# Kernel optimization log

Hardware: AMD Instinct MI355X
Metric: run time of the kernel (lower is better)

Reference implementation:

```python
import jax, jax.numpy as jnp
import numpy as np

Na, Nn, E, D = 8192, 65536, 262144, 128
NB = 2  # n_blk Att blocks
EPS = 1e-5  # torch GroupNorm default eps


def _gn(x, g, b):
    # GroupNorm with 1 group on [N, C]: normalize each row over channels
    mu = jnp.mean(x, axis=-1, keepdims=True)
    var = jnp.mean((x - mu) ** 2, axis=-1, keepdims=True)
    return (x - mu) * jax.lax.rsqrt(var + EPS) * g + b


def setup_inputs() -> dict:
    key = jax.random.key(0)
    ks = jax.random.split(key, 28)
    s = 0.05
    inp = {
        'actors': jax.random.normal(ks[0], (Na, D), jnp.float32),
        'nodes': jax.random.normal(ks[1], (Nn, D), jnp.float32),
        'actor_ctrs': jax.random.uniform(ks[2], (Na, 2), jnp.float32, 0.0, 100.0),
        'node_ctrs': jax.random.uniform(ks[3], (Nn, 2), jnp.float32, 0.0, 100.0),
        'hi': jax.random.randint(ks[4], (E,), 0, Na, jnp.int32),
        'wi': jax.random.randint(ks[5], (E,), 0, Nn, jnp.int32),
        # stacked params for NB=2 Att blocks
        'dist0_W': jax.random.normal(ks[6], (NB, D, 2), jnp.float32) * s,
        'dist0_b': jnp.zeros((NB, D), jnp.float32),
        'dist1_W': jax.random.normal(ks[7], (NB, D, D), jnp.float32) * s,
        'dist1_g': jnp.ones((NB, D), jnp.float32),
        'dist1_b': jnp.zeros((NB, D), jnp.float32),
        'query_W': jax.random.normal(ks[8], (NB, D, D), jnp.float32) * s,
        'query_g': jnp.ones((NB, D), jnp.float32),
        'query_b': jnp.zeros((NB, D), jnp.float32),
        'ctx0_W': jax.random.normal(ks[9], (NB, D, 3 * D), jnp.float32) * s,
        'ctx0_g': jnp.ones((NB, D), jnp.float32),
        'ctx0_b': jnp.zeros((NB, D), jnp.float32),
        'ctx1_W': jax.random.normal(ks[10], (NB, D, D), jnp.float32) * s,
        'agt_W': jax.random.normal(ks[11], (NB, D, D), jnp.float32) * s,
        'norm_g': jnp.ones((NB, D), jnp.float32),
        'norm_b': jnp.zeros((NB, D), jnp.float32),
        'lin_W': jax.random.normal(ks[12], (NB, D, D), jnp.float32) * s,
        'lin_g': jnp.ones((NB, D), jnp.float32),
        'lin_b': jnp.zeros((NB, D), jnp.float32),
    }
    return inp


def reference(actors, nodes, actor_ctrs, node_ctrs, hi, wi,
              dist0_W, dist0_b, dist1_W, dist1_g, dist1_b,
              query_W, query_g, query_b,
              ctx0_W, ctx0_g, ctx0_b, ctx1_W, agt_W,
              norm_g, norm_b, lin_W, lin_g, lin_b):
    for i in range(NB):
        res = actors
        # dist MLP on edge displacement vectors [E, 2]
        d = actor_ctrs[hi] - node_ctrs[wi]
        d = jax.nn.relu(d @ dist0_W[i].T + dist0_b[i])
        d = jax.nn.relu(_gn(d @ dist1_W[i].T, dist1_g[i], dist1_b[i]))
        # query from target agents, gathered per-edge
        q = jax.nn.relu(_gn(actors @ query_W[i].T, query_g[i], query_b[i]))[hi]
        c = nodes[wi]
        m = jnp.concatenate([d, q, c], axis=-1)  # [E, 3D]
        m = jax.nn.relu(_gn(m @ ctx0_W[i].T, ctx0_g[i], ctx0_b[i]))
        m = m @ ctx1_W[i].T  # [E, D]
        # scatter-add messages into agents (index_add_)
        a = actors @ agt_W[i].T
        a = a.at[hi].add(m)
        a = jax.nn.relu(_gn(a, norm_g[i], norm_b[i]))
        a = _gn(a @ lin_W[i].T, lin_g[i], lin_b[i])  # act=False
        actors = jax.nn.relu(a + res)
    return actors
```

## Files before the change

kernel.cpp:

```cpp
#include <hip/hip_runtime.h>
#include <hip/hip_bf16.h>

typedef __hip_bfloat16 bf16;
typedef __attribute__((ext_vector_type(8))) short bf16x8;
typedef __attribute__((ext_vector_type(4))) float f32x4;

constexpr int DD = 128;
constexpr int NAC = 8192;
constexpr int NND = 65536;
constexpr int NEG = 262144;
constexpr int AP = 136;
constexpr float GN_EPS = 1e-5f;

#define DEVINL __device__ __attribute__((always_inline)) static inline

DEVINL float bf2f(short s) {
    return __uint_as_float(((unsigned int)(unsigned short)s) << 16);
}

DEVINL void stage_half(const bf16* __restrict__ src, bf16* buf, int wid, int lane)
{
    const bf16* g = src + (size_t)(wid * 4) * 512 + lane * 8;
    bf16* l = buf + (wid * 4) * 512;
    #pragma unroll
    for (int i = 0; i < 4; i++) {
        __builtin_amdgcn_global_load_lds(
            (const __attribute__((address_space(1))) void*)(g + i * 512),
            (__attribute__((address_space(3))) void*)(l + i * 512),
            16, 0, 0);
    }
}

DEVINL void stage_h16(const bf16* __restrict__ src, bf16* buf, int lane)
{
    const bf16* g = src + lane * 8;
    #pragma unroll
    for (int i = 0; i < 16; i++) {
        __builtin_amdgcn_global_load_lds(
            (const __attribute__((address_space(1))) void*)(g + i * 512),
            (__attribute__((address_space(3))) void*)(buf + i * 512),
            16, 0, 0);
    }
}

DEVINL void compute_half(const bf16* buf, const bf16* Abuf,
                         f32x4 (&acc)[2][8], int eb, int quad, int l16, int lane, int kh)
{
    #pragma unroll
    for (int ks2 = 0; ks2 < 2; ks2++) {
        int kk = kh + ks2 * 32;
        bf16x8 a0 = *(const bf16x8*)(Abuf + (eb + l16) * AP + kk + quad * 8);
        bf16x8 a1 = *(const bf16x8*)(Abuf + (eb + 16 + l16) * AP + kk + quad * 8);
        #pragma unroll
        for (int nt = 0; nt < 8; nt++) {
            bf16x8 b = *(const bf16x8*)(buf + ((ks2 * 8 + nt) * 64 + lane) * 8);
            acc[0][nt] = __builtin_amdgcn_mfma_f32_16x16x32_bf16(a0, b, acc[0][nt], 0, 0, 0);
            acc[1][nt] = __builtin_amdgcn_mfma_f32_16x16x32_bf16(a1, b, acc[1][nt], 0, 0, 0);
        }
    }
}

DEVINL void zero_acc(f32x4 (&acc)[2][8])
{
    #pragma unroll
    for (int i = 0; i < 2; i++)
        #pragma unroll
        for (int j = 0; j < 8; j++)
            acc[i][j] = f32x4{0.f, 0.f, 0.f, 0.f};
}

DEVINL void gn_relu_to_lds(f32x4 (&acc)[2][8], const float* __restrict__ g,
                           const float* __restrict__ b, bf16* Abuf,
                           int eb, int quad, int l16)
{
    float gv[8], bv[8];
    #pragma unroll
    for (int nt = 0; nt < 8; nt++) { gv[nt] = g[nt * 16 + l16]; bv[nt] = b[nt * 16 + l16]; }
    #pragma unroll
    for (int mt = 0; mt < 2; mt++) {
        #pragma unroll
        for (int r = 0; r < 4; r++) {
            float s1 = 0.f, s2 = 0.f;
            #pragma unroll
            for (int nt = 0; nt < 8; nt++) { float v = acc[mt][nt][r]; s1 += v; s2 += v * v; }
            #pragma unroll
            for (int m = 1; m < 16; m <<= 1) { s1 += __shfl_xor(s1, m, 64); s2 += __shfl_xor(s2, m, 64); }
            float mean = s1 * (1.f / 128.f);
            float sc = rsqrtf(s2 * (1.f / 128.f) - mean * mean + GN_EPS);
            int row = eb + mt * 16 + quad * 4 + r;
            #pragma unroll
            for (int nt = 0; nt < 8; nt++) {
                float y = (acc[mt][nt][r] - mean) * sc * gv[nt] + bv[nt];
                Abuf[row * AP + nt * 16 + l16] = __float2bfloat16(fmaxf(y, 0.f));
            }
        }
    }
}

DEVINL void gn_relu_acc(f32x4 (&acc)[2][8], const float* __restrict__ g,
                        const float* __restrict__ b, int l16)
{
    float gv[8], bv[8];
    #pragma unroll
    for (int nt = 0; nt < 8; nt++) { gv[nt] = g[nt * 16 + l16]; bv[nt] = b[nt * 16 + l16]; }
    #pragma unroll
    for (int mt = 0; mt < 2; mt++) {
        #pragma unroll
        for (int r = 0; r < 4; r++) {
            float s1 = 0.f, s2 = 0.f;
            #pragma unroll
            for (int nt = 0; nt < 8; nt++) { float v = acc[mt][nt][r]; s1 += v; s2 += v * v; }
            #pragma unroll
            for (int m = 1; m < 16; m <<= 1) { s1 += __shfl_xor(s1, m, 64); s2 += __shfl_xor(s2, m, 64); }
            float mean = s1 * (1.f / 128.f);
            float sc = rsqrtf(s2 * (1.f / 128.f) - mean * mean + GN_EPS);
            #pragma unroll
            for (int nt = 0; nt < 8; nt++)
                acc[mt][nt][r] = fmaxf((acc[mt][nt][r] - mean) * sc * gv[nt] + bv[nt], 0.f);
        }
    }
}

DEVINL bf16x8 pack_row(const f32x4 (&acc)[2][8], int mt, int r)
{
    union { bf16x8 v; bf16 h[8]; } u;
    #pragma unroll
    for (int nt = 0; nt < 8; nt++) u.h[nt] = __float2bfloat16(acc[mt][nt][r]);
    return u.v;
}

__global__ void repack_w_kernel(const float* __restrict__ d1, const float* __restrict__ qw,
                                const float* __restrict__ c0, const float* __restrict__ c1,
                                const float* __restrict__ ag, const float* __restrict__ li,
                                bf16* __restrict__ Wf, int* __restrict__ cnt)
{
    int g = blockIdx.x * 256 + threadIdx.x;
    if (g < 8192) cnt[g] = 0;
    int slice = g >> 11;
    int t = g & 2047;
    int i = slice >> 3;
    int sid = slice & 7;
    int lane = t & 63, nt = (t >> 6) & 7, ks = t >> 9;
    const float* src; int stride = 128, koff = 0;
    switch (sid) {
        case 0:  src = d1 + i * 16384; break;
        case 1:  src = qw + i * 16384; break;
        case 2:  src = c0 + i * 49152; stride = 384; koff = 0;   break;
        case 3:  src = c0 + i * 49152; stride = 384; koff = 128; break;
        case 4:  src = c0 + i * 49152; stride = 384; koff = 256; break;
        case 5:  src = c1 + i * 16384; break;
        case 6:  src = ag + i * 16384; break;
        default: src = li + i * 16384; break;
    }
    int n = nt * 16 + (lane & 15);
    int k = ks * 32 + (lane >> 4) * 8;
    const float* p = src + (size_t)n * stride + koff + k;
    float4 v0 = *(const float4*)(p);
    float4 v1 = *(const float4*)(p + 4);
    union { bf16x8 v; bf16 h[8]; } u;
    u.h[0] = __float2bfloat16(v0.x); u.h[1] = __float2bfloat16(v0.y);
    u.h[2] = __float2bfloat16(v0.z); u.h[3] = __float2bfloat16(v0.w);
    u.h[4] = __float2bfloat16(v1.x); u.h[5] = __float2bfloat16(v1.y);
    u.h[6] = __float2bfloat16(v1.z); u.h[7] = __float2bfloat16(v1.w);
    *(bf16x8*)(Wf + (size_t)slice * 16384 + (size_t)t * 8) = u.v;
}

__global__ void hist_kernel(const int* __restrict__ hi, int* __restrict__ cnt)
{
    int e = blockIdx.x * blockDim.x + threadIdx.x;
    atomicAdd(&cnt[hi[e]], 1);
}

__global__ void scan_kernel(const int* __restrict__ cnt, int* __restrict__ cur)
{
    __shared__ int part[1024];
    int t = threadIdx.x;
    int local[8]; int s = 0;
    #pragma unroll
    for (int k = 0; k < 8; k++) { local[k] = cnt[t * 8 + k]; s += local[k]; }
    part[t] = s;
    __syncthreads();
    for (int d = 1; d < 1024; d <<= 1) {
        int v = (t >= d) ? part[t - d] : 0;
        __syncthreads();
        part[t] += v;
        __syncthreads();
    }
    int base = t ? part[t - 1] : 0;
    #pragma unroll
    for (int k = 0; k < 8; k++) { cur[t * 8 + k] = base; base += local[k]; }
}

__global__ void scatter_kernel(const int* __restrict__ hi, const int* __restrict__ wi,
                               const float* __restrict__ actor_ctrs, const float* __restrict__ node_ctrs,
                               int* __restrict__ cur,
                               int* __restrict__ hi_s, int* __restrict__ wi_s,
                               float2* __restrict__ dxy_s)
{
    int e = blockIdx.x * blockDim.x + threadIdx.x;
    int h = hi[e], w = wi[e];
    int p = atomicAdd(&cur[h], 1);
    hi_s[p] = h; wi_s[p] = w;
    float2 a2 = ((const float2*)actor_ctrs)[h];
    float2 n2 = ((const float2*)node_ctrs)[w];
    dxy_s[p] = float2{a2.x - n2.x, a2.y - n2.y};
}

__global__ __launch_bounds__(256, 3) void nodec_kernel(
    const float* __restrict__ nodes, const bf16* __restrict__ c0cf, bf16* __restrict__ nc)
{
    __shared__ __align__(16) bf16 Abuf[128 * AP];
    __shared__ __align__(16) bf16 Wd[8192];
    int tid = threadIdx.x, wid = tid >> 6, lane = tid & 63, quad = lane >> 4, l16 = lane & 15;
    int eb = wid * 32, r0 = blockIdx.x * 128;
    stage_half(c0cf, Wd, wid, lane);
    for (int rr = 0; rr < 32; rr++) {
        int row = r0 + eb + rr;
        float2 v = ((const float2*)(nodes + (size_t)row * DD))[lane];
        __hip_bfloat162 p; p.x = __float2bfloat16(v.x); p.y = __float2bfloat16(v.y);
        *(__hip_bfloat162*)(Abuf + (eb + rr) * AP + lane * 2) = p;
    }
    f32x4 acc[2][8]; zero_acc(acc);
    __syncthreads();
    compute_half(Wd, Abuf, acc, eb, quad, l16, lane, 0);
    __syncthreads();
    stage_half(c0cf + 8192, Wd, wid, lane);
    __syncthreads();
    compute_half(Wd, Abuf, acc, eb, quad, l16, lane, 64);
    #pragma unroll
    for (int mt = 0; mt < 2; mt++)
        #pragma unroll
        for (int r = 0; r < 4; r++) {
            int row = r0 + eb + mt * 16 + quad * 4 + r;
            *(bf16x8*)(nc + (size_t)row * DD + l16 * 8) = pack_row(acc, mt, r);
        }
}

__global__ __launch_bounds__(64) void prep_kernel(
    const float* __restrict__ actors_in,
    const bf16* __restrict__ agf, const bf16* __restrict__ qwf,
    const float* __restrict__ qg, const float* __restrict__ qb,
    const bf16* __restrict__ c0qf,
    bf16* __restrict__ qc, float* __restrict__ A_acc, float* __restrict__ M_acc)
{
    __shared__ __align__(16) bf16 Abuf[32 * AP];
    __shared__ __align__(16) bf16 Wd[8192];
    int lane = threadIdx.x, quad = lane >> 4, l16 = lane & 15;
    int r0 = blockIdx.x * 32;
    stage_h16(agf, Wd, lane);
    for (int rr = 0; rr < 32; rr++) {
        float2 v = ((const float2*)(actors_in + (size_t)(r0 + rr) * DD))[lane];
        __hip_bfloat162 p; p.x = __float2bfloat16(v.x); p.y = __float2bfloat16(v.y);
        *(__hip_bfloat162*)(Abuf + rr * AP + lane * 2) = p;
    }
    #pragma unroll
    for (int rr = 0; rr < 16; rr++) {
        int row = r0 + rr * 2 + (lane >> 5);
        ((float4*)(M_acc + (size_t)row * DD))[lane & 31] = float4{0.f, 0.f, 0.f, 0.f};
    }
    f32x4 acc[2][8];
    zero_acc(acc);
    __syncthreads();
    compute_half(Wd, Abuf, acc, 0, quad, l16, lane, 0);
    __syncthreads();
    stage_h16(agf + 8192, Wd, lane);
    __syncthreads();
    compute_half(Wd, Abuf, acc, 0, quad, l16, lane, 64);
    __syncthreads();
    stage_h16(qwf, Wd, lane);
    #pragma unroll
    for (int mt = 0; mt < 2; mt++)
        #pragma unroll
        for (int r = 0; r < 4; r++) {
            int row = r0 + mt * 16 + quad * 4 + r;
            float4 w0{acc[mt][0][r], acc[mt][1][r], acc[mt][2][r], acc[mt][3][r]};
            float4 w1{acc[mt][4][r], acc[mt][5][r], acc[mt][6][r], acc[mt][7][r]};
            float4* p = (float4*)(A_acc + (size_t)row * DD + l16 * 8);
            p[0] = w0; p[1] = w1;
        }
    zero_acc(acc);
    __syncthreads();
    compute_half(Wd, Abuf, acc, 0, quad, l16, lane, 0);
    __syncthreads();
    stage_h16(qwf + 8192, Wd, lane);
    __syncthreads();
    compute_half(Wd, Abuf, acc, 0, quad, l16, lane, 64);
    __syncthreads();
    stage_h16(c0qf, Wd, lane);
    gn_relu_to_lds(acc, qg, qb, Abuf, 0, quad, l16);
    zero_acc(acc);
    __syncthreads();
    compute_half(Wd, Abuf, acc, 0, quad, l16, lane, 0);
    __syncthreads();
    stage_h16(c0qf + 8192, Wd, lane);
    __syncthreads();
    compute_half(Wd, Abuf, acc, 0, quad, l16, lane, 64);
    #pragma unroll
    for (int mt = 0; mt < 2; mt++)
        #pragma unroll
        for (int r = 0; r < 4; r++) {
            int row = r0 + mt * 16 + quad * 4 + r;
            *(bf16x8*)(qc + (size_t)row * DD + l16 * 8) = pack_row(acc, mt, r);
        }
}

__global__ __launch_bounds__(256, 3) void edge_kernel(
    const int* __restrict__ hi_s, const int* __restrict__ wi_s, const float2* __restrict__ dxy_s,
    const float* __restrict__ d0W, const float* __restrict__ d0b,
    const bf16* __restrict__ d1f, const float* __restrict__ d1g, const float* __restrict__ d1bb,
    const bf16* __restrict__ qc, const bf16* __restrict__ nc,
    const bf16* __restrict__ c0df, const float* __restrict__ c0g, const float* __restrict__ c0bb,
    float* __restrict__ M_acc)
{
    __shared__ __align__(16) bf16 Abuf[128 * AP];
    __shared__ __align__(16) bf16 Wd[8192];
    __shared__ float2 dxy[4][32];
    int tid = threadIdx.x, wid = tid >> 6, lane = tid & 63, quad = lane >> 4, l16 = lane & 15;
    int eb = wid * 32, e0 = blockIdx.x * 128 + eb;

    stage_half(d1f, Wd, wid, lane);

    int hrows[2][4], wrows[2][4];
    #pragma unroll
    for (int mt = 0; mt < 2; mt++)
        #pragma unroll
        for (int r = 0; r < 4; r++) {
            int e = e0 + mt * 16 + quad * 4 + r;
            hrows[mt][r] = hi_s[e];
            wrows[mt][r] = wi_s[e];
        }

    if (lane < 32) dxy[wid][lane] = dxy_s[e0 + lane];
    {
        int ch = lane * 2;
        float w00 = d0W[ch * 2], w01 = d0W[ch * 2 + 1], bb0 = d0b[ch];
        float w10 = d0W[ch * 2 + 2], w11 = d0W[ch * 2 + 3], bb1 = d0b[ch + 1];
        #pragma unroll
        for (int rr = 0; rr < 32; rr++) {
            float2 d = dxy[wid][rr];
            float y0 = fmaxf(d.x * w00 + d.y * w01 + bb0, 0.f);
            float y1 = fmaxf(d.x * w10 + d.y * w11 + bb1, 0.f);
            __hip_bfloat162 p; p.x = __float2bfloat16(y0); p.y = __float2bfloat16(y1);
            *(__hip_bfloat162*)(Abuf + (eb + rr) * AP + ch) = p;
        }
    }
    f32x4 acc[2][8];

    zero_acc(acc);
    __syncthreads();
    compute_half(Wd, Abuf, acc, eb, quad, l16, lane, 0);
    __syncthreads();
    stage_half(d1f + 8192, Wd, wid, lane);
    __syncthreads();
    compute_half(Wd, Abuf, acc, eb, quad, l16, lane, 64);
    __syncthreads();
    stage_half(c0df, Wd, wid, lane);
    gn_relu_to_lds(acc, d1g, d1bb, Abuf, eb, quad, l16);

    #pragma unroll
    for (int mt = 0; mt < 2; mt++) {
        bf16x8 qv[4], nv[4];
        #pragma unroll
        for (int r = 0; r < 4; r++) {
            qv[r] = *(const bf16x8*)(qc + (size_t)hrows[mt][r] * DD + l16 * 8);
            nv[r] = *(const bf16x8*)(nc + (size_t)wrows[mt][r] * DD + l16 * 8);
        }
        #pragma unroll
        for (int r = 0; r < 4; r++)
            #pragma unroll
            for (int nt = 0; nt < 8; nt++)
                acc[mt][nt][r] = bf2f(qv[r][nt]) + bf2f(nv[r][nt]);
    }
    __syncthreads();
    compute_half(Wd, Abuf, acc, eb, quad, l16, lane, 0);
    __syncthreads();
    stage_half(c0df + 8192, Wd, wid, lane);
    __syncthreads();
    compute_half(Wd, Abuf, acc, eb, quad, l16, lane, 64);

    gn_relu_acc(acc, c0g, c0bb, l16);
    #pragma unroll
    for (int mt = 0; mt < 2; mt++) {
        int h0 = hrows[mt][0];
        int href = __shfl(h0, 0, 64);
        bool same = (hrows[mt][0] == href) && (hrows[mt][1] == href) &&
                    (hrows[mt][2] == href) && (hrows[mt][3] == href);
        if (__all(same)) {
            float s[8];
            #pragma unroll
            for (int nt = 0; nt < 8; nt++) {
                s[nt] = acc[mt][nt][0] + acc[mt][nt][1] + acc[mt][nt][2] + acc[mt][nt][3];
                s[nt] += __shfl_xor(s[nt], 16, 64);
                s[nt] += __shfl_xor(s[nt], 32, 64);
            }
            if (quad == 0) {
                float* dst = M_acc + (size_t)href * DD + l16;
                #pragma unroll
                for (int nt = 0; nt < 8; nt++) atomicAdd(dst + nt * 16, s[nt]);
            }
        } else {
            float run[8];
            int curh = hrows[mt][0];
            #pragma unroll
            for (int nt = 0; nt < 8; nt++) run[nt] = acc[mt][nt][0];
            #pragma unroll
            for (int r = 1; r < 4; r++) {
                int hr = hrows[mt][r];
                if (hr == curh) {
                    #pragma unroll
                    for (int nt = 0; nt < 8; nt++) run[nt] += acc[mt][nt][r];
                } else {
                    float* dst = M_acc + (size_t)curh * DD + l16;
                    #pragma unroll
                    for (int nt = 0; nt < 8; nt++) atomicAdd(dst + nt * 16, run[nt]);
                    curh = hr;
                    #pragma unroll
                    for (int nt = 0; nt < 8; nt++) run[nt] = acc[mt][nt][r];
                }
            }
            float* dst = M_acc + (size_t)curh * DD + l16;
            #pragma unroll
            for (int nt = 0; nt < 8; nt++) atomicAdd(dst + nt * 16, run[nt]);
        }
    }
}

__global__ __launch_bounds__(64) void post_kernel(
    const float* __restrict__ A_acc,
    const float* __restrict__ M_acc,
    const bf16* __restrict__ c1f,
    const float* __restrict__ ng, const float* __restrict__ nb,
    const bf16* __restrict__ lif, const float* __restrict__ lg, const float* __restrict__ lb,
    const float* __restrict__ resid, float* __restrict__ outp)
{
    __shared__ __align__(16) bf16 Ahi[32 * AP];
    __shared__ __align__(16) bf16 Alo[32 * AP];
    __shared__ __align__(16) bf16 Wd[8192];
    int lane = threadIdx.x, quad = lane >> 4, l16 = lane & 15;
    int r0 = blockIdx.x * 32;

    stage_h16(c1f, Wd, lane);
    for (int rr = 0; rr < 32; rr++) {
        float2 x = ((const float2*)(M_acc + (size_t)(r0 + rr) * DD))[lane];
        bf16 h0 = __float2bfloat16(x.x), h1 = __float2bfloat16(x.y);
        float l0 = x.x - __bfloat162float(h0), l1 = x.y - __bfloat162float(h1);
        __hip_bfloat162 ph; ph.x = h0; ph.y = h1;
        __hip_bfloat162 pl; pl.x = __float2bfloat16(l0); pl.y = __float2bfloat16(l1);
        *(__hip_bfloat162*)(Ahi + rr * AP + lane * 2) = ph;
        *(__hip_bfloat162*)(Alo + rr * AP + lane * 2) = pl;
    }
    f32x4 acc[2][8]; zero_acc(acc);
    __syncthreads();
    compute_half(Wd, Ahi, acc, 0, quad, l16, lane, 0);
    compute_half(Wd, Alo, acc, 0, quad, l16, lane, 0);
    __syncthreads();
    stage_h16(c1f + 8192, Wd, lane);
    __syncthreads();
    compute_half(Wd, Ahi, acc, 0, quad, l16, lane, 64);
    compute_half(Wd, Alo, acc, 0, quad, l16, lane, 64);
    #pragma unroll
    for (int mt = 0; mt < 2; mt++)
        #pragma unroll
        for (int r = 0; r < 4; r++) {
            int row = r0 + mt * 16 + quad * 4 + r;
            const float4* p = (const float4*)(A_acc + (size_t)row * DD + l16 * 8);
            float4 v0 = p[0], v1 = p[1];
            acc[mt][0][r] += v0.x; acc[mt][1][r] += v0.y;
            acc[mt][2][r] += v0.z; acc[mt][3][r] += v0.w;
            acc[mt][4][r] += v1.x; acc[mt][5][r] += v1.y;
            acc[mt][6][r] += v1.z; acc[mt][7][r] += v1.w;
        }
    __syncthreads();
    stage_h16(lif, Wd, lane);
    gn_relu_to_lds(acc, ng, nb, Ahi, 0, quad, l16);
    f32x4 acc2[2][8]; zero_acc(acc2);
    __syncthreads();
    compute_half(Wd, Ahi, acc2, 0, quad, l16, lane, 0);
    __syncthreads();
    stage_h16(lif + 8192, Wd, lane);
    __syncthreads();
    compute_half(Wd, Ahi, acc2, 0, quad, l16, lane, 64);

    float gv[8], bv[8];
    #pragma unroll
    for (int nt = 0; nt < 8; nt++) { gv[nt] = lg[nt * 16 + l16]; bv[nt] = lb[nt * 16 + l16]; }
    #pragma unroll
    for (int mt = 0; mt < 2; mt++)
        #pragma unroll
        for (int r = 0; r < 4; r++) {
            float s1 = 0.f, s2 = 0.f;
            #pragma unroll
            for (int nt = 0; nt < 8; nt++) { float v = acc2[mt][nt][r]; s1 += v; s2 += v * v; }
            #pragma unroll
            for (int m = 1; m < 16; m <<= 1) { s1 += __shfl_xor(s1, m, 64); s2 += __shfl_xor(s2, m, 64); }
            float mean = s1 * (1.f / 128.f);
            float sc = rsqrtf(s2 * (1.f / 128.f) - mean * mean + GN_EPS);
            int row = r0 + mt * 16 + quad * 4 + r;
            #pragma unroll
            for (int nt = 0; nt < 8; nt++) {
                float y = (acc2[mt][nt][r] - mean) * sc * gv[nt] + bv[nt];
                size_t o = (size_t)row * DD + nt * 16 + l16;
                outp[o] = fmaxf(y + resid[o], 0.f);
            }
        }
}

extern "C" void kernel_launch(void* const* d_in, const int* in_sizes, int n_in,
                              void* d_out, int out_size, void* d_ws, size_t ws_size,
                              hipStream_t stream)
{
    const float* actors     = (const float*)d_in[0];
    const float* nodes      = (const float*)d_in[1];
    const float* actor_ctrs = (const float*)d_in[2];
    const float* node_ctrs  = (const float*)d_in[3];
    const int*   hi         = (const int*)d_in[4];
    const int*   wi         = (const int*)d_in[5];
    const float* dist0_W    = (const float*)d_in[6];
    const float* dist0_b    = (const float*)d_in[7];
    const float* dist1_W    = (const float*)d_in[8];
    const float* dist1_g    = (const float*)d_in[9];
    const float* dist1_b    = (const float*)d_in[10];
    const float* query_W    = (const float*)d_in[11];
    const float* query_g    = (const float*)d_in[12];
    const float* query_b    = (const float*)d_in[13];
    const float* ctx0_W     = (const float*)d_in[14];
    const float* ctx0_g     = (const float*)d_in[15];
    const float* ctx0_b     = (const float*)d_in[16];
    const float* ctx1_W     = (const float*)d_in[17];
    const float* agt_W      = (const float*)d_in[18];
    const float* norm_g     = (const float*)d_in[19];
    const float* norm_b     = (const float*)d_in[20];
    const float* lin_W      = (const float*)d_in[21];
    const float* lin_g      = (const float*)d_in[22];
    const float* lin_b      = (const float*)d_in[23];

    char* ws = (char*)d_ws;
    size_t off = 0;
    bf16*  Wf         = (bf16*)(ws + off);  off += 524288;
    float* A_acc      = (float*)(ws + off); off += 4194304;
    float* M_acc      = (float*)(ws + off); off += 4194304;
    float* actors_mid = (float*)(ws + off); off += 4194304;
    bf16*  qc_bf      = (bf16*)(ws + off);  off += 2097152;
    bf16*  nc_bf      = (bf16*)(ws + off);  off += 16777216;
    int*   cnt        = (int*)(ws + off);   off += 32768;
    int*   cur        = (int*)(ws + off);   off += 32768;
    int*   hi_s       = (int*)(ws + off);   off += 1048576;
    int*   wi_s       = (int*)(ws + off);   off += 1048576;
    float2* dxy_s     = (float2*)(ws + off); off += 2097152;

    repack_w_kernel<<<128, 256, 0, stream>>>(dist1_W, query_W, ctx0_W, ctx1_W, agt_W, lin_W,
                                             Wf, cnt);

    hist_kernel<<<NEG / 256, 256, 0, stream>>>(hi, cnt);
    scan_kernel<<<1, 1024, 0, stream>>>(cnt, cur);
    scatter_kernel<<<NEG / 256, 256, 0, stream>>>(hi, wi, actor_ctrs, node_ctrs,
                                                  cur, hi_s, wi_s, dxy_s);

    for (int i = 0; i < 2; i++) {
        const bf16* d1f  = Wf + (size_t)(i * 8 + 0) * 16384;
        const bf16* qwf  = Wf + (size_t)(i * 8 + 1) * 16384;
        const bf16* c0df = Wf + (size_t)(i * 8 + 2) * 16384;
        const bf16* c0qf = Wf + (size_t)(i * 8 + 3) * 16384;
        const bf16* c0cf = Wf + (size_t)(i * 8 + 4) * 16384;
        const bf16* c1f  = Wf + (size_t)(i * 8 + 5) * 16384;
        const bf16* agf  = Wf + (size_t)(i * 8 + 6) * 16384;
        const bf16* lif  = Wf + (size_t)(i * 8 + 7) * 16384;
        const float* curp = i ? actors_mid : actors;
        float* nxt = i ? (float*)d_out : actors_mid;

        nodec_kernel<<<NND / 128, 256, 0, stream>>>(nodes, c0cf, nc_bf);
        prep_kernel<<<NAC / 32, 64, 0, stream>>>(curp, agf, qwf,
            query_g + i * 128, query_b + i * 128, c0qf, qc_bf, A_acc, M_acc);
        edge_kernel<<<NEG / 128, 256, 0, stream>>>(hi_s, wi_s, dxy_s,
            dist0_W + i * 256, dist0_b + i * 128,
            d1f, dist1_g + i * 128, dist1_b + i * 128,
            qc_bf, nc_bf, c0df, ctx0_g + i * 128, ctx0_b + i * 128, M_acc);
        post_kernel<<<NAC / 32, 64, 0, stream>>>(A_acc, M_acc, c1f,
            norm_g + i * 128, norm_b + i * 128,
            lif, lin_g + i * 128, lin_b + i * 128, curp, nxt);
    }
}
```

Measured before the change: 350.7 us.

## Pre-convert nodes to padded bf16 once and DMA them into LDS; merge per-wave scatter atomics

Adds a one-time kernel that converts the fp32 nodes to a padded bf16 layout, which both blocks then share. The nodec kernel loads that layout straight into LDS with global_load_lds, replacing the per-row fp32 loads and in-kernel conversion. The edge kernel's scatter first checks whether all 32 rows of a wave share one target agent and, if so, issues a single set of atomics instead of one per 16-row tile. The cost is an extra ~17 MB workspace buffer and a conversion pass whose traffic is only paid back across the two blocks.

```diff
diff --git a/kernel.cpp b/kernel.cpp
--- a/kernel.cpp
+++ b/kernel.cpp
@@ -165,6 +165,17 @@
     *(bf16x8*)(Wf + (size_t)slice * 16384 + (size_t)t * 8) = u.v;
 }
 
+__global__ void nodes_conv_kernel(const float* __restrict__ nodes, bf16* __restrict__ nbp)
+{
+    int g = blockIdx.x * 256 + threadIdx.x;
+    int row = g >> 5;
+    int c4 = (g & 31) * 4;
+    float4 v = *(const float4*)(nodes + (size_t)row * DD + c4);
+    bf16* d = nbp + (size_t)row * AP + c4;
+    d[0] = __float2bfloat16(v.x); d[1] = __float2bfloat16(v.y);
+    d[2] = __float2bfloat16(v.z); d[3] = __float2bfloat16(v.w);
+}
+
 __global__ void hist_kernel(const int* __restrict__ hi, int* __restrict__ cnt)
 {
     int e = blockIdx.x * blockDim.x + threadIdx.x;
@@ -207,18 +218,25 @@
 }
 
 __global__ __launch_bounds__(256, 3) void nodec_kernel(
-    const float* __restrict__ nodes, const bf16* __restrict__ c0cf, bf16* __restrict__ nc)
+    const bf16* __restrict__ nbp, const bf16* __restrict__ c0cf, bf16* __restrict__ nc)
 {
     __shared__ __align__(16) bf16 Abuf[128 * AP];
     __shared__ __align__(16) bf16 Wd[8192];
     int tid = threadIdx.x, wid = tid >> 6, lane = tid & 63, quad = lane >> 4, l16 = lane & 15;
     int eb = wid * 32, r0 = blockIdx.x * 128;
     stage_half(c0cf, Wd, wid, lane);
-    for (int rr = 0; rr < 32; rr++) {
-        int row = r0 + eb + rr;
-        float2 v = ((const float2*)(nodes + (size_t)row * DD))[lane];
-        __hip_bfloat162 p; p.x = __float2bfloat16(v.x); p.y = __float2bfloat16(v.y);
-        *(__hip_bfloat162*)(Abuf + (eb + rr) * AP + lane * 2) = p;
+    {
+        const bf16* src = nbp + (size_t)r0 * AP;
+        #pragma unroll
+        for (int i = 0; i < 9; i++) {
+            int idx = i * 256 + tid;
+            if (idx < 2176) {
+                __builtin_amdgcn_global_load_lds(
+                    (const __attribute__((address_space(1))) void*)(src + idx * 8),
+                    (__attribute__((address_space(3))) void*)(Abuf + idx * 8),
+                    16, 0, 0);
+            }
+        }
     }
     f32x4 acc[2][8]; zero_acc(acc);
     __syncthreads();
@@ -379,17 +397,19 @@
     compute_half(Wd, Abuf, acc, eb, quad, l16, lane, 64);
 
     gn_relu_acc(acc, c0g, c0bb, l16);
-    #pragma unroll
-    for (int mt = 0; mt < 2; mt++) {
-        int h0 = hrows[mt][0];
-        int href = __shfl(h0, 0, 64);
-        bool same = (hrows[mt][0] == href) && (hrows[mt][1] == href) &&
-                    (hrows[mt][2] == href) && (hrows[mt][3] == href);
-        if (__all(same)) {
+    {
+        int href = __shfl(hrows[0][0], 0, 64);
+        bool sameAll = true;
+        #pragma unroll
+        for (int mt = 0; mt < 2; mt++)
+            #pragma unroll
+            for (int r = 0; r < 4; r++) sameAll = sameAll && (hrows[mt][r] == href);
+        if (__all(sameAll)) {
             float s[8];
             #pragma unroll
             for (int nt = 0; nt < 8; nt++) {
-                s[nt] = acc[mt][nt][0] + acc[mt][nt][1] + acc[mt][nt][2] + acc[mt][nt][3];
+                s[nt] = acc[0][nt][0] + acc[0][nt][1] + acc[0][nt][2] + acc[0][nt][3]
+                      + acc[1][nt][0] + acc[1][nt][1] + acc[1][nt][2] + acc[1][nt][3];
                 s[nt] += __shfl_xor(s[nt], 16, 64);
                 s[nt] += __shfl_xor(s[nt], 32, 64);
             }
@@ -399,28 +419,49 @@
                 for (int nt = 0; nt < 8; nt++) atomicAdd(dst + nt * 16, s[nt]);
             }
         } else {
-            float run[8];
-            int curh = hrows[mt][0];
-            #pragma unroll
-            for (int nt = 0; nt < 8; nt++) run[nt] = acc[mt][nt][0];
-            #pragma unroll
-            for (int r = 1; r < 4; r++) {
-                int hr = hrows[mt][r];
-                if (hr == curh) {
+            #pragma unroll
+            for (int mt = 0; mt < 2; mt++) {
+                int hrefm = __shfl(hrows[mt][0], 0, 64);
+                bool same = (hrows[mt][0] == hrefm) && (hrows[mt][1] == hrefm) &&
+                            (hrows[mt][2] == hrefm) && (hrows[mt][3] == hrefm);
+                if (__all(same)) {
+                    float s[8];
                     #pragma unroll
-                    for (int nt = 0; nt < 8; nt++) run[nt] += acc[mt][nt][r];
+                    for (int nt = 0; nt < 8; nt++) {
+                        s[nt] = acc[mt][nt][0] + acc[mt][nt][1] + acc[mt][nt][2] + acc[mt][nt][3];
+                        s[nt] += __shfl_xor(s[nt], 16, 64);
+                        s[nt] += __shfl_xor(s[nt], 32, 64);
+                    }
+                    if (quad == 0) {
+                        float* dst = M_acc + (size_t)hrefm * DD + l16;
+                        #pragma unroll
+                        for (int nt = 0; nt < 8; nt++) atomicAdd(dst + nt * 16, s[nt]);
+                    }
                 } else {
+                    float run[8];
+                    int curh = hrows[mt][0];
+                    #pragma unroll
+                    for (int nt = 0; nt < 8; nt++) run[nt] = acc[mt][nt][0];
+                    #pragma unroll
+                    for (int r = 1; r < 4; r++) {
+                        int hr = hrows[mt][r];
+                        if (hr == curh) {
+                            #pragma unroll
+                            for (int nt = 0; nt < 8; nt++) run[nt] += acc[mt][nt][r];
+                        } else {
+                            float* dst = M_acc + (size_t)curh * DD + l16;
+                            #pragma unroll
+                            for (int nt = 0; nt < 8; nt++) atomicAdd(dst + nt * 16, run[nt]);
+                            curh = hr;
+                            #pragma unroll
+                            for (int nt = 0; nt < 8; nt++) run[nt] = acc[mt][nt][r];
+                        }
+                    }
                     float* dst = M_acc + (size_t)curh * DD + l16;
                     #pragma unroll
                     for (int nt = 0; nt < 8; nt++) atomicAdd(dst + nt * 16, run[nt]);
-                    curh = hr;
-                    #pragma unroll
-                    for (int nt = 0; nt < 8; nt++) run[nt] = acc[mt][nt][r];
                 }
             }
-            float* dst = M_acc + (size_t)curh * DD + l16;
-            #pragma unroll
-            for (int nt = 0; nt < 8; nt++) atomicAdd(dst + nt * 16, run[nt]);
         }
     }
 }
@@ -542,6 +583,7 @@
     float* actors_mid = (float*)(ws + off); off += 4194304;
     bf16*  qc_bf      = (bf16*)(ws + off);  off += 2097152;
     bf16*  nc_bf      = (bf16*)(ws + off);  off += 16777216;
+    bf16*  nodes_bfp  = (bf16*)(ws + off);  off += 17825792;
     int*   cnt        = (int*)(ws + off);   off += 32768;
     int*   cur        = (int*)(ws + off);   off += 32768;
     int*   hi_s       = (int*)(ws + off);   off += 1048576;
@@ -550,6 +592,7 @@
 
     repack_w_kernel<<<128, 256, 0, stream>>>(dist1_W, query_W, ctx0_W, ctx1_W, agt_W, lin_W,
                                              Wf, cnt);
+    nodes_conv_kernel<<<NND * 32 / 256, 256, 0, stream>>>(nodes, nodes_bfp);
 
     hist_kernel<<<NEG / 256, 256, 0, stream>>>(hi, cnt);
     scan_kernel<<<1, 1024, 0, stream>>>(cnt, cur);
@@ -568,7 +611,7 @@
         const float* curp = i ? actors_mid : actors;
         float* nxt = i ? (float*)d_out : actors_mid;
 
-        nodec_kernel<<<NND / 128, 256, 0, stream>>>(nodes, c0cf, nc_bf);
+        nodec_kernel<<<NND / 128, 256, 0, stream>>>(nodes_bfp, c0cf, nc_bf);
         prep_kernel<<<NAC / 32, 64, 0, stream>>>(curp, agf, qwf,
             query_g + i * 128, query_b + i * 128, c0qf, qc_bf, A_acc, M_acc);
         edge_kernel<<<NEG / 128, 256, 0, stream>>>(hi_s, wi_s, dxy_s,
```

Measured after the change: 359.8 us. 2.6% more time.
